# Optimization experiments

Measured on AMD Instinct MI355X. Metric: run time of the kernel, lower is better.

## Reference

```python
import jax, jax.numpy as jnp
import numpy as np

B, H, S, DH = 2, 16, 2048, 64

def setup_inputs() -> dict:
    key = jax.random.key(0)
    k1, k2, k3 = jax.random.split(key, 3)
    return {
        "query": jax.random.normal(k1, (B, H, S, DH), dtype=jnp.float32),
        "key": jax.random.normal(k2, (B, H, S, DH), dtype=jnp.float32),
        "value": jax.random.normal(k3, (B, H, S, DH), dtype=jnp.float32),
        "key_padding_mask": jnp.zeros((B, S), dtype=bool),
    }

def reference(query, key, value, key_padding_mask):
    # scores: [B, H, Sq, Sk]
    scale = 1.0 / jnp.sqrt(jnp.asarray(query.shape[-1], query.dtype))
    scores = jnp.einsum("bhqd,bhkd->bhqk", query, key) * scale
    # key padding mask broadcasts over heads and query positions
    scores = jnp.where(key_padding_mask[:, None, None, :], -jnp.inf, scores)
    attn = jax.nn.softmax(scores, axis=-1)
    # dropout is identity in eval mode (deterministic reference)
    out = jnp.einsum("bhqk,bhkd->bhqd", attn, value)
    # [B, H, S, Dh] -> [B, S, H*Dh]
    b, h, s, dh = out.shape
    return out.transpose(0, 2, 1, 3).reshape(b, s, h * dh)
```

## Files before the change

kernel.cpp:

```cpp
#include <hip/hip_runtime.h>

typedef __attribute__((ext_vector_type(4))) float f32x4;
typedef __attribute__((ext_vector_type(4))) short s16x4;
typedef __attribute__((ext_vector_type(8))) short s16x8;

constexpr int Bn = 2, Hn = 16, Sn = 2048, DHn = 64;
constexpr int TQ = 64;
constexpr int TK = 64;
constexpr int NT = Sn / TK;
constexpr int TILE_SH = TK * DHn;
constexpr float SHIFT = 16.0f;

__device__ __forceinline__ unsigned pk2(float a, float b) {
  unsigned ua = __builtin_bit_cast(unsigned, a);
  unsigned ub = __builtin_bit_cast(unsigned, b);
  ua += 0x7fffu + ((ua >> 16) & 1u);
  ub += 0x7fffu + ((ub >> 16) & 1u);
  return (ua >> 16) | (ub & 0xffff0000u);
}

__device__ __forceinline__ float fexp2(float x) {
#if __has_builtin(__builtin_amdgcn_exp2f)
  return __builtin_amdgcn_exp2f(x);
#else
  return exp2f(x);
#endif
}

__device__ __forceinline__ void gl2lds16(const short* g, short* l) {
  __builtin_amdgcn_global_load_lds(
      (const __attribute__((address_space(1))) void*)g,
      (__attribute__((address_space(3))) void*)l, 16, 0, 0);
}

__global__ __launch_bounds__(256, 4)
void prepack_kernel(const float* __restrict__ Kg, const float* __restrict__ Vg,
                    short* __restrict__ Kp, short* __restrict__ Vp) {
  const int blk = blockIdx.x;
  const int tid = threadIdx.x;
  const float* Kt = Kg + (size_t)blk * TILE_SH;
  const float* Vt = Vg + (size_t)blk * TILE_SH;
  short* Kd = Kp + (size_t)blk * TILE_SH;
  short* Vd = Vp + (size_t)blk * TILE_SH;

  {
    const int r = tid >> 2;
    const int cb = (tid & 3) * 2;
#pragma unroll
    for (int cc = 0; cc < 2; ++cc) {
      int c = cb + cc;
      const float4* p = (const float4*)(Kt + (size_t)r * DHn + c * 8);
      float4 x = p[0], y = p[1];
      union { unsigned u[4]; s16x8 v; } tmp;
      tmp.u[0] = pk2(x.x, x.y); tmp.u[1] = pk2(x.z, x.w);
      tmp.u[2] = pk2(y.x, y.y); tmp.u[3] = pk2(y.z, y.w);
      *(s16x8*)&Kd[r * 64 + (c ^ (r & 7)) * 8] = tmp.v;
    }
  }
  {
    const int d = tid & 63;
    const int kb = (tid >> 6) * 16;
#pragma unroll
    for (int cc = 0; cc < 2; ++cc) {
      int k0 = kb + cc * 8;
      float v0[8];
#pragma unroll
      for (int j = 0; j < 8; ++j) v0[j] = Vt[(size_t)(k0 + j) * DHn + d];
      union { unsigned u[4]; s16x8 v; } tmp;
      tmp.u[0] = pk2(v0[0], v0[1]); tmp.u[1] = pk2(v0[2], v0[3]);
      tmp.u[2] = pk2(v0[4], v0[5]); tmp.u[3] = pk2(v0[6], v0[7]);
      int c = k0 >> 3;
      *(s16x8*)&Vd[d * 64 + (c ^ (d & 7)) * 8] = tmp.v;
    }
  }
}

__global__ __launch_bounds__(128, 2)
void fattn_kernel(const float* __restrict__ Qg, const short* __restrict__ Kp,
                  const short* __restrict__ Vp, const unsigned char* __restrict__ maskg,
                  float* __restrict__ Og) {
  __shared__ __align__(16) short Ksh[TILE_SH];
  __shared__ __align__(16) short VTsh[TILE_SH];
  __shared__ __align__(16) short Psh[2 * 32 * 64];
  __shared__ __align__(16) float Mb[TK];

  const int tid  = threadIdx.x;
  const int w    = tid >> 6;
  const int lane = tid & 63;
  const int n    = lane & 15;
  const int q4   = lane >> 4;
  const int swz  = n & 7;

  const int blk = blockIdx.x;
  const int bh  = blk & 31;
  const int qt  = blk >> 5;
  const int b   = bh >> 4;
  const int h   = bh & 15;

  const float* Qb = Qg + (size_t)bh * Sn * DHn;
  const short* Kt = Kp + (size_t)bh * NT * TILE_SH;
  const short* Vt = Vp + (size_t)bh * NT * TILE_SH;
  const unsigned char* mq = maskg + (size_t)b * Sn;

  const int q0 = qt * TQ + w * 32;

  const float c1 = 0.125f * 1.4426950408889634f;
  s16x8 qf[2][2];
#pragma unroll
  for (int qg = 0; qg < 2; ++qg) {
    const float* qrow = Qb + (size_t)(q0 + qg * 16 + n) * DHn;
#pragma unroll
    for (int kc = 0; kc < 2; ++kc) {
      const float4* p = (const float4*)(qrow + kc * 32 + q4 * 8);
      float4 x = p[0], y = p[1];
      union { unsigned u[4]; s16x8 v; } tmp;
      tmp.u[0] = pk2(x.x * c1, x.y * c1);
      tmp.u[1] = pk2(x.z * c1, x.w * c1);
      tmp.u[2] = pk2(y.x * c1, y.y * c1);
      tmp.u[3] = pk2(y.z * c1, y.w * c1);
      qf[qg][kc] = tmp.v;
    }
  }

  const int c0   = q4 ^ swz;
  const int offA = n * 64 + c0 * 8;
  const int offB = n * 64 + (c0 ^ 4) * 8;
  const int prowA = (w * 32 + n) * 64;
  const int pc   = (q4 >> 1) ^ swz;
  const int pwo  = (q4 & 1) * 4;

  f32x4 Oa[2][4];
#pragma unroll
  for (int qg = 0; qg < 2; ++qg)
#pragma unroll
    for (int na = 0; na < 4; ++na) Oa[qg][na] = (f32x4){0.f, 0.f, 0.f, 0.f};
  float lsum[2] = {0.f, 0.f};

  for (int t = 0; t < NT; ++t) {
    __syncthreads();

#pragma unroll
    for (int k = 0; k < 4; ++k) {
      gl2lds16(Kt + k * 1024 + tid * 8, &Ksh[k * 1024 + w * 512]);
      gl2lds16(Vt + k * 1024 + tid * 8, &VTsh[k * 1024 + w * 512]);
    }
    if (tid < TK) Mb[tid] = mq[t * TK + tid] ? -1e30f : -SHIFT;
    __syncthreads();

    s16x8 kf[4][2];
#pragma unroll
    for (int mc = 0; mc < 4; ++mc) {
      kf[mc][0] = *(const s16x8*)&Ksh[mc * 1024 + offA];
      kf[mc][1] = *(const s16x8*)&Ksh[mc * 1024 + offB];
    }
    f32x4 bias[4];
#pragma unroll
    for (int mc = 0; mc < 4; ++mc)
      bias[mc] = *(const f32x4*)&Mb[mc * 16 + q4 * 4];

#pragma unroll
    for (int qg = 0; qg < 2; ++qg) {
      f32x4 sa[4];
#pragma unroll
      for (int mc = 0; mc < 4; ++mc) sa[mc] = bias[mc];
#pragma unroll
      for (int mc = 0; mc < 4; ++mc)
#pragma unroll
        for (int kc = 0; kc < 2; ++kc)
          sa[mc] = __builtin_amdgcn_mfma_f32_16x16x32_bf16(kf[mc][kc], qf[qg][kc], sa[mc], 0, 0, 0);

      const int prow = prowA + qg * (16 * 64);
      float ls = 0.f;
#pragma unroll
      for (int mc = 0; mc < 4; ++mc) {
        float p0 = fexp2(sa[mc][0]);
        float p1 = fexp2(sa[mc][1]);
        float p2 = fexp2(sa[mc][2]);
        float p3 = fexp2(sa[mc][3]);
        ls += (p0 + p1) + (p2 + p3);
        union { unsigned u[2]; s16x4 v4; } pw;
        pw.u[0] = pk2(p0, p1);
        pw.u[1] = pk2(p2, p3);
        *(s16x4*)&Psh[prow + ((pc ^ (2 * mc)) * 8) + pwo] = pw.v4;
      }
      ls += __shfl_xor(ls, 16);
      ls += __shfl_xor(ls, 32);
      lsum[qg] += ls;
    }

    s16x8 vf[4][2];
#pragma unroll
    for (int na = 0; na < 4; ++na) {
      vf[na][0] = *(const s16x8*)&VTsh[na * 1024 + offA];
      vf[na][1] = *(const s16x8*)&VTsh[na * 1024 + offB];
    }
#pragma unroll
    for (int qg = 0; qg < 2; ++qg) {
      const int prow = prowA + qg * (16 * 64);
      s16x8 pf[2];
      pf[0] = *(const s16x8*)&Psh[prow + ((q4 ^ swz) * 8)];
      pf[1] = *(const s16x8*)&Psh[prow + (((4 + q4) ^ swz) * 8)];
#pragma unroll
      for (int na = 0; na < 4; ++na)
#pragma unroll
        for (int kc = 0; kc < 2; ++kc)
          Oa[qg][na] = __builtin_amdgcn_mfma_f32_16x16x32_bf16(pf[kc], vf[na][kc], Oa[qg][na], 0, 0, 0);
    }

    Kt += TILE_SH;
    Vt += TILE_SH;
  }

#pragma unroll
  for (int qg = 0; qg < 2; ++qg) {
#pragma unroll
    for (int r = 0; r < 4; ++r) {
      float lr  = __shfl(lsum[qg], q4 * 4 + r);
      float inv = 1.0f / lr;
      int q = q0 + qg * 16 + q4 * 4 + r;
      float* orow = Og + (size_t)(b * Sn + q) * (Hn * DHn) + h * DHn;
#pragma unroll
      for (int na = 0; na < 4; ++na)
        orow[na * 16 + n] = Oa[qg][na][r] * inv;
    }
  }
}

extern "C" void kernel_launch(void* const* d_in, const int* in_sizes, int n_in,
                              void* d_out, int out_size, void* d_ws, size_t ws_size,
                              hipStream_t stream) {
  (void)in_sizes; (void)n_in; (void)ws_size; (void)out_size;
  const float* Q = (const float*)d_in[0];
  const float* K = (const float*)d_in[1];
  const float* V = (const float*)d_in[2];
  const unsigned char* mask = (const unsigned char*)d_in[3];
  float* out = (float*)d_out;

  short* Kp = (short*)d_ws;
  short* Vp = Kp + (size_t)Bn * Hn * Sn * DHn;

  hipLaunchKernelGGL(prepack_kernel, dim3(Bn * Hn * NT), dim3(256), 0, stream, K, V, Kp, Vp);
  hipLaunchKernelGGL(fattn_kernel, dim3(Bn * Hn * (Sn / TQ)), dim3(128), 0, stream,
                     Q, Kp, Vp, mask, out);
}
```

Before: 156.0 us.

## Double-buffer K tiles, overlap V loads with QK, read mask into registers

K tiles are now double-buffered in LDS, so the next tile is prefetched while the current one is used. The V tile load is issued before the QK^T MFMAs, and the barriers are moved so V is only awaited before the PV stage. The mask is read directly into registers and prefetched one tile ahead, which removes the shared Mb buffer. The per-tile cross-lane lsum reduction is deferred to the epilogue, and s_setprio brackets the MFMA bursts. LDS use grows by one K tile, and the loop still has two barriers per iteration.

```diff
diff --git a/kernel.cpp b/kernel.cpp
--- a/kernel.cpp
+++ b/kernel.cpp
@@ -79,10 +79,9 @@
 void fattn_kernel(const float* __restrict__ Qg, const short* __restrict__ Kp,
                   const short* __restrict__ Vp, const unsigned char* __restrict__ maskg,
                   float* __restrict__ Og) {
-  __shared__ __align__(16) short Ksh[TILE_SH];
-  __shared__ __align__(16) short VTsh[TILE_SH];
+  __shared__ __align__(16) short Ksh[2][TILE_SH];
+  __shared__ __align__(16) short Vsh[TILE_SH];
   __shared__ __align__(16) short Psh[2 * 32 * 64];
-  __shared__ __align__(16) float Mb[TK];
 
   const int tid  = threadIdx.x;
   const int w    = tid >> 6;
@@ -136,38 +135,62 @@
     for (int na = 0; na < 4; ++na) Oa[qg][na] = (f32x4){0.f, 0.f, 0.f, 0.f};
   float lsum[2] = {0.f, 0.f};
 
+#pragma unroll
+  for (int k = 0; k < 4; ++k)
+    gl2lds16(Kt + k * 1024 + tid * 8, &Ksh[0][k * 1024 + w * 512]);
+  unsigned m4[4];
+#pragma unroll
+  for (int mc = 0; mc < 4; ++mc)
+    m4[mc] = *(const unsigned*)&mq[mc * 16 + q4 * 4];
+  __syncthreads();
+
+  int nb = 0;
   for (int t = 0; t < NT; ++t) {
-    __syncthreads();
-
-#pragma unroll
-    for (int k = 0; k < 4; ++k) {
-      gl2lds16(Kt + k * 1024 + tid * 8, &Ksh[k * 1024 + w * 512]);
-      gl2lds16(Vt + k * 1024 + tid * 8, &VTsh[k * 1024 + w * 512]);
-    }
-    if (tid < TK) Mb[tid] = mq[t * TK + tid] ? -1e30f : -SHIFT;
-    __syncthreads();
+    f32x4 bias[4];
+#pragma unroll
+    for (int mc = 0; mc < 4; ++mc)
+#pragma unroll
+      for (int r = 0; r < 4; ++r)
+        bias[mc][r] = ((m4[mc] >> (8 * r)) & 0xffu) ? -1e30f : -SHIFT;
+
+    if (t + 1 < NT) {
+#pragma unroll
+      for (int mc = 0; mc < 4; ++mc)
+        m4[mc] = *(const unsigned*)&mq[(t + 1) * TK + mc * 16 + q4 * 4];
+    }
+
+    {
+      const short* Vg = Vt + (size_t)t * TILE_SH;
+#pragma unroll
+      for (int k = 0; k < 4; ++k)
+        gl2lds16(Vg + k * 1024 + tid * 8, &Vsh[k * 1024 + w * 512]);
+    }
+    if (t + 1 < NT) {
+      const short* Kg2 = Kt + (size_t)(t + 1) * TILE_SH;
+#pragma unroll
+      for (int k = 0; k < 4; ++k)
+        gl2lds16(Kg2 + k * 1024 + tid * 8, &Ksh[nb ^ 1][k * 1024 + w * 512]);
+    }
 
     s16x8 kf[4][2];
 #pragma unroll
     for (int mc = 0; mc < 4; ++mc) {
-      kf[mc][0] = *(const s16x8*)&Ksh[mc * 1024 + offA];
-      kf[mc][1] = *(const s16x8*)&Ksh[mc * 1024 + offB];
-    }
-    f32x4 bias[4];
-#pragma unroll
-    for (int mc = 0; mc < 4; ++mc)
-      bias[mc] = *(const f32x4*)&Mb[mc * 16 + q4 * 4];
+      kf[mc][0] = *(const s16x8*)&Ksh[nb][mc * 1024 + offA];
+      kf[mc][1] = *(const s16x8*)&Ksh[nb][mc * 1024 + offB];
+    }
 
 #pragma unroll
     for (int qg = 0; qg < 2; ++qg) {
       f32x4 sa[4];
 #pragma unroll
       for (int mc = 0; mc < 4; ++mc) sa[mc] = bias[mc];
+      __builtin_amdgcn_s_setprio(1);
 #pragma unroll
       for (int mc = 0; mc < 4; ++mc)
 #pragma unroll
         for (int kc = 0; kc < 2; ++kc)
           sa[mc] = __builtin_amdgcn_mfma_f32_16x16x32_bf16(kf[mc][kc], qf[qg][kc], sa[mc], 0, 0, 0);
+      __builtin_amdgcn_s_setprio(0);
 
       const int prow = prowA + qg * (16 * 64);
       float ls = 0.f;
@@ -183,16 +206,16 @@
         pw.u[1] = pk2(p2, p3);
         *(s16x4*)&Psh[prow + ((pc ^ (2 * mc)) * 8) + pwo] = pw.v4;
       }
-      ls += __shfl_xor(ls, 16);
-      ls += __shfl_xor(ls, 32);
       lsum[qg] += ls;
     }
 
+    __syncthreads();
+
     s16x8 vf[4][2];
 #pragma unroll
     for (int na = 0; na < 4; ++na) {
-      vf[na][0] = *(const s16x8*)&VTsh[na * 1024 + offA];
-      vf[na][1] = *(const s16x8*)&VTsh[na * 1024 + offB];
+      vf[na][0] = *(const s16x8*)&Vsh[na * 1024 + offA];
+      vf[na][1] = *(const s16x8*)&Vsh[na * 1024 + offB];
     }
 #pragma unroll
     for (int qg = 0; qg < 2; ++qg) {
@@ -200,17 +223,24 @@
       s16x8 pf[2];
       pf[0] = *(const s16x8*)&Psh[prow + ((q4 ^ swz) * 8)];
       pf[1] = *(const s16x8*)&Psh[prow + (((4 + q4) ^ swz) * 8)];
+      __builtin_amdgcn_s_setprio(1);
 #pragma unroll
       for (int na = 0; na < 4; ++na)
 #pragma unroll
         for (int kc = 0; kc < 2; ++kc)
           Oa[qg][na] = __builtin_amdgcn_mfma_f32_16x16x32_bf16(pf[kc], vf[na][kc], Oa[qg][na], 0, 0, 0);
-    }
-
-    Kt += TILE_SH;
-    Vt += TILE_SH;
-  }
-
+      __builtin_amdgcn_s_setprio(0);
+    }
+
+    __syncthreads();
+    nb ^= 1;
+  }
+
+#pragma unroll
+  for (int qg = 0; qg < 2; ++qg) {
+    lsum[qg] += __shfl_xor(lsum[qg], 16);
+    lsum[qg] += __shfl_xor(lsum[qg], 32);
+  }
 #pragma unroll
   for (int qg = 0; qg < 2; ++qg) {
 #pragma unroll
```

New measurement: 155.4 us. Within noise of the previous version (-0.4%).
